# Kernel tuning notes

Hardware: AMD Instinct MI355X
Metric: run time of the kernel (lower is better)

## Reference

```python
import jax, jax.numpy as jnp
import numpy as np

BN_EPS = 1e-5
R = 8.0        # radius
L = 11         # sequence kernel size (odd), s = L//2
K = 24         # kernel_channels[-1]
N_NODES = 32768
N_EDGES = 524288
C_IN = 128     # in_channels == out_channels
C_W = 32       # width = out_channels * base_width / 64


def _bn(x, gamma, beta):
    # BatchNorm1d in training mode: biased batch statistics over node dim
    mu = jnp.mean(x, axis=0)
    var = jnp.mean(jnp.square(x - mu), axis=0)
    return (x - mu) * jax.lax.rsqrt(var + BN_EPS) * gamma + beta


def _lrelu(x, slope):
    return jnp.where(x >= 0, x, slope * x)


def setup_inputs() -> dict:
    key = jax.random.key(0)
    ks = jax.random.split(key, 10)

    def glorot(k, shape, fan_in):
        return jax.random.normal(k, shape, jnp.float32) * np.float32(1.0 / np.sqrt(fan_in))

    inp = {}
    inp["x"] = jax.random.normal(ks[0], (N_NODES, C_IN), jnp.float32)
    inp["pos"] = jax.random.normal(ks[1], (N_NODES, 3), jnp.float32) * 10.0
    inp["ori"] = jax.random.normal(ks[2], (N_NODES, 9), jnp.float32)
    inp["seq"] = jnp.arange(N_NODES, dtype=jnp.int32)
    inp["edge_index"] = jax.random.randint(ks[3], (2, N_EDGES), 0, N_NODES, jnp.int32)
    # input MLP params: BN(C_IN) -> LeakyReLU(0.1) -> Linear(C_IN->C_W, no bias) -> BN(C_W) -> LeakyReLU(0.1)
    inp["bn1_g"] = jnp.ones((C_IN,), jnp.float32)
    inp["bn1_b"] = jnp.zeros((C_IN,), jnp.float32)
    inp["lin1_w"] = glorot(ks[4], (C_IN, C_W), C_IN)
    inp["bn2_g"] = jnp.ones((C_W,), jnp.float32)
    inp["bn2_b"] = jnp.zeros((C_W,), jnp.float32)
    # CDConv WeightNet (single layer kernel_channels=[K]): per-seq-bin affine 7 -> K
    inp["wn_w"] = glorot(ks[5], (L, 7, K), 7)
    inp["wn_b"] = jnp.zeros((L, K), jnp.float32)
    # CDConv output projection: [K*C_W, C_W]
    inp["conv_w"] = glorot(ks[6], (K * C_W, C_W), K * C_W)
    # output Linear: BN(C_W) -> LeakyReLU(0.1) -> Linear(C_W->C_IN, no bias)
    inp["bn3_g"] = jnp.ones((C_W,), jnp.float32)
    inp["bn3_b"] = jnp.zeros((C_W,), jnp.float32)
    inp["lin2_w"] = glorot(ks[7], (C_W, C_IN), C_W)
    return inp


def reference(x, pos, ori, seq, edge_index,
              bn1_g, bn1_b, lin1_w, bn2_g, bn2_b,
              wn_w, wn_b, conv_w, bn3_g, bn3_b, lin2_w):
    n = x.shape[0]
    identity = x  # in_channels == out_channels -> identity branch is passthrough

    # ----- input MLP (mid_channels=None) -----
    h = _lrelu(_bn(x, bn1_g, bn1_b), 0.1)
    h = h @ lin1_w                       # [N, C_W]
    h = _lrelu(_bn(h, bn2_g, bn2_b), 0.1)

    # ----- CDConv: continuous geometric kernel over neighbor edges -----
    src, dst = edge_index[0], edge_index[1]      # message j=src -> i=dst
    d = pos[src] - pos[dst]                      # [E,3]
    dist = jnp.linalg.norm(d, axis=-1, keepdims=True)
    direction = d / (dist + 1e-9)
    Ri = ori[dst].reshape(-1, 3, 3)              # receiver local frame
    Rj = ori[src].reshape(-1, 3, 3)
    pos_local = jnp.einsum('eij,ej->ei', Ri, direction)      # direction in local frame
    ori_feat = jnp.einsum('eij,ej->ei', Ri, Rj[:, 0, :])     # neighbor axis in local frame
    delta = jnp.concatenate([pos_local, ori_feat, dist / R], axis=-1)  # [E,7]

    s = L // 2
    sidx = jnp.clip(seq[src] - seq[dst], -s, s) + s          # [E] in [0, L)

    # WeightNet: per-edge affine selected by sequence bin, LeakyReLU(0.2)
    w = _lrelu(jnp.einsum('ef,efk->ek', delta, wn_w[sidx]) + wn_b[sidx], 0.2)  # [E,K]

    # message = outer(kernel_weight, x_j), scatter-sum to receivers
    msg = (w[:, :, None] * h[src][:, None, :]).reshape(w.shape[0], K * C_W)   # [E, K*C_W]
    agg = jax.ops.segment_sum(msg, dst, num_segments=n)                        # [N, K*C_W]
    h = agg @ conv_w                                                            # [N, C_W]

    # ----- output Linear + residual -----
    h = _lrelu(_bn(h, bn3_g, bn3_b), 0.1)
    out = h @ lin2_w + identity
    return out
```

## Files before the change

kernel.cpp:

```cpp
#include <hip/hip_runtime.h>

#define N_NODES 32768
#define C_IN 128
#define C_W 32
#define KK 24
#define SS 5
#define NPB 8
#define TC 256
#define AGS (KK * C_W + 4)
#define WNS 172
#define WBS 28
#define HS 36

#define BF_LO(u) __uint_as_float((u) << 16)
#define BF_HI(u) __uint_as_float((u) & 0xFFFF0000u)

__device__ __forceinline__ unsigned int bf16pair(float lo, float hi) {
    unsigned int ulo = __float_as_uint(lo);
    unsigned int uhi = __float_as_uint(hi);
    ulo = (ulo + 0x7FFFu + ((ulo >> 16) & 1u)) >> 16;
    uhi = (uhi + 0x7FFFu + ((uhi >> 16) & 1u)) & 0xFFFF0000u;
    return uhi | ulo;
}

__global__ void __launch_bounds__(256) k_pre(
        const float* __restrict__ x, float* __restrict__ s1,
        const int* __restrict__ ei, int E, int* __restrict__ counts) {
    int t = threadIdx.x;
    int c = t % C_IN;
    int r0 = blockIdx.x * 2 + t / C_IN;
    float s = 0.f, sq = 0.f;
    for (int r = r0; r < N_NODES; r += 1024) {
        float v = x[(size_t)r * C_IN + c];
        s += v; sq += v * v;
    }
    atomicAdd(&s1[c], s);
    atomicAdd(&s1[C_IN + c], sq);
    for (int e = blockIdx.x * 256 + t; e < E; e += 512 * 256)
        atomicAdd(&counts[ei[E + e]], 1);
}

__global__ void __launch_bounds__(256) k_mlp1(
        const float* __restrict__ x, const float* __restrict__ s1,
        const float* __restrict__ g1, const float* __restrict__ b1,
        const float* __restrict__ w1, float* __restrict__ hpre,
        float* __restrict__ s2sh) {
    __shared__ float sAB[2][C_IN];
    __shared__ float sx[32][C_IN + 4];
    __shared__ float sw[C_IN][C_W];
    const int t = threadIdx.x;
    const int row0 = blockIdx.x * 32;
    if (t < C_IN) {
        float mean = s1[t] * (1.f / N_NODES);
        float var = s1[C_IN + t] * (1.f / N_NODES) - mean * mean;
        float a = g1[t] * rsqrtf(var + 1e-5f);
        sAB[0][t] = a; sAB[1][t] = b1[t] - mean * a;
    }
    for (int idx = t; idx < C_IN * C_W; idx += 256)
        sw[idx / C_W][idx % C_W] = w1[idx];
    __syncthreads();
    for (int idx = t; idx < 32 * 32; idx += 256) {
        int r = idx >> 5, cq = idx & 31;
        float4 v = *(const float4*)&x[(size_t)(row0 + r) * C_IN + cq * 4];
        float* d = &sx[r][cq * 4];
        float a0 = sAB[0][cq*4+0]*v.x + sAB[1][cq*4+0];
        float a1 = sAB[0][cq*4+1]*v.y + sAB[1][cq*4+1];
        float a2 = sAB[0][cq*4+2]*v.z + sAB[1][cq*4+2];
        float a3 = sAB[0][cq*4+3]*v.w + sAB[1][cq*4+3];
        d[0] = a0 >= 0.f ? a0 : 0.1f * a0;
        d[1] = a1 >= 0.f ? a1 : 0.1f * a1;
        d[2] = a2 >= 0.f ? a2 : 0.1f * a2;
        d[3] = a3 >= 0.f ? a3 : 0.1f * a3;
    }
    __syncthreads();
    const int r = t >> 3, c0 = (t & 7) * 4;
    float ac0 = 0.f, ac1 = 0.f, ac2 = 0.f, ac3 = 0.f;
    #pragma unroll 8
    for (int cc = 0; cc < C_IN; ++cc) {
        float xv = sx[r][cc];
        float4 wv = *(const float4*)&sw[cc][c0];
        ac0 += xv * wv.x; ac1 += xv * wv.y; ac2 += xv * wv.z; ac3 += xv * wv.w;
    }
    float4 o; o.x = ac0; o.y = ac1; o.z = ac2; o.w = ac3;
    *(float4*)&hpre[(size_t)(row0 + r) * C_W + c0] = o;
    __syncthreads();
    sx[r][c0] = ac0; sx[r][c0+1] = ac1; sx[r][c0+2] = ac2; sx[r][c0+3] = ac3;
    __syncthreads();
    if (t < C_W) {
        float s = 0.f, sq = 0.f;
        #pragma unroll
        for (int rr = 0; rr < 32; ++rr) {
            float v = sx[rr][t];
            s += v; sq += v * v;
        }
        int sh = (blockIdx.x & 7) * 64;
        atomicAdd(&s2sh[sh + t], s);
        atomicAdd(&s2sh[sh + C_W + t], sq);
    }
}

__global__ void __launch_bounds__(1024) k_scan(
        const int* __restrict__ counts, int* __restrict__ offsets,
        int* __restrict__ cursor) {
    __shared__ int sblk[1024];
    const int t = threadIdx.x;
    const int base = t * 32;
    const int4* cp = (const int4*)(counts + base);
    int loc[32];
    int s = 0;
    #pragma unroll
    for (int q = 0; q < 8; ++q) {
        int4 v = cp[q];
        loc[q*4+0] = s; s += v.x;
        loc[q*4+1] = s; s += v.y;
        loc[q*4+2] = s; s += v.z;
        loc[q*4+3] = s; s += v.w;
    }
    sblk[t] = s;
    __syncthreads();
    for (int d = 1; d < 1024; d <<= 1) {
        int u = (t >= d) ? sblk[t - d] : 0;
        __syncthreads();
        sblk[t] += u;
        __syncthreads();
    }
    const int blockbase = sblk[t] - s;
    #pragma unroll
    for (int q = 0; q < 8; ++q) {
        int4 o;
        o.x = blockbase + loc[q*4+0];
        o.y = blockbase + loc[q*4+1];
        o.z = blockbase + loc[q*4+2];
        o.w = blockbase + loc[q*4+3];
        ((int4*)(offsets + base))[q] = o;
        ((int4*)(cursor + base))[q] = o;
    }
    if (t == 1023) offsets[N_NODES] = sblk[1023];
}

__global__ void __launch_bounds__(256) k_scatter(
        const int* __restrict__ ei, int E, int* __restrict__ cursor,
        int* __restrict__ srcPerm) {
    int e = blockIdx.x * 256 + threadIdx.x;
    if (e < E) {
        int dst = ei[E + e];
        int p = atomicAdd(&cursor[dst], 1);
        srcPerm[p] = ei[e];
    }
}

__global__ void __launch_bounds__(512) k_mega(
    const int* __restrict__ offsets, const int* __restrict__ srcPerm,
    const float* __restrict__ pos, const float* __restrict__ ori,
    const int* __restrict__ seq, const float* __restrict__ hpre,
    const float* __restrict__ s2sh, const float* __restrict__ g2,
    const float* __restrict__ b2,
    const float* __restrict__ wnw, const float* __restrict__ wnb,
    const float* __restrict__ convw,
    float* __restrict__ convout, float* __restrict__ s3sh) {

    __shared__ float sWnw[11 * WNS];
    __shared__ float sWnb[11 * WBS];
    __shared__ float sA2[C_W], sB2[C_W];
    __shared__ int   sOff[NPB + 1];
    __shared__ float sNd[NPB][13];
    __shared__ union SU {
        struct { unsigned short h[TC * HS]; unsigned int w[TC * 12]; } stg;
        struct { float agg[NPB][AGS]; float red[8][NPB][C_W];
                 float rv[NPB][C_W]; float rq[NPB][C_W]; } fin;
    } U;

    const int t = threadIdx.x;
    const int i0 = blockIdx.x * NPB;
    for (int idx = t; idx < 11 * 168; idx += 512)
        sWnw[(idx / 168) * WNS + idx % 168] = wnw[idx];
    for (int idx = t; idx < 11 * 24; idx += 512)
        sWnb[(idx / 24) * WBS + idx % 24] = wnb[idx];
    if (t < C_W) {
        float s = 0.f, sq = 0.f;
        #pragma unroll
        for (int j = 0; j < 8; ++j) {
            s  += s2sh[j * 64 + t];
            sq += s2sh[j * 64 + C_W + t];
        }
        float mean = s * (1.f / N_NODES);
        float var = sq * (1.f / N_NODES) - mean * mean;
        float a = g2[t] * rsqrtf(var + 1e-5f);
        sA2[t] = a; sB2[t] = b2[t] - mean * a;
    }
    if (t <= NPB) sOff[t] = offsets[i0 + t];
    if (t < NPB * 13) {
        int n = t / 13, f = t % 13;
        float v;
        if (f < 3)       v = pos[(i0 + n) * 3 + f];
        else if (f < 12) v = ori[(i0 + n) * 9 + (f - 3)];
        else             v = __int_as_float(seq[i0 + n]);
        sNd[n][f] = v;
    }
    __syncthreads();

    const int w = t >> 6, lane = t & 63, c = lane & 31, s = lane >> 5;
    const int beg = sOff[w], end = sOff[w + 1];
    const int blkBeg = sOff[0], blkEnd = sOff[NPB];
    float a[KK];
    #pragma unroll
    for (int k = 0; k < KK; ++k) a[k] = 0.f;

    for (int base = blkBeg; base < blkEnd; base += TC) {
        const int cnt = min(TC, blkEnd - base);
        __syncthreads();
        {
            const int e    = t & 255;
            const int half = t >> 8;
            if (e < cnt) {
                const int slot = base + e;
                int g = 0;
                #pragma unroll
                for (int j = 1; j < NPB; ++j) g += (slot >= sOff[j]);
                const int src = srcPerm[slot];
                float px = pos[src*3+0], py = pos[src*3+1], pz = pos[src*3+2];
                float o0 = ori[src*9+0], o1 = ori[src*9+1], o2 = ori[src*9+2];
                int sqs = seq[src];
                float dx = px - sNd[g][0], dy = py - sNd[g][1], dz = pz - sNd[g][2];
                float dist = sqrtf(dx*dx + dy*dy + dz*dz);
                float inv = 1.f / (dist + 1e-9f);
                float ux = dx*inv, uy = dy*inv, uz = dz*inv;
                float df[7];
                #pragma unroll
                for (int r = 0; r < 3; ++r) {
                    float m0 = sNd[g][3 + r*3 + 0];
                    float m1 = sNd[g][3 + r*3 + 1];
                    float m2 = sNd[g][3 + r*3 + 2];
                    df[r]     = m0*ux + m1*uy + m2*uz;
                    df[3 + r] = m0*o0 + m1*o1 + m2*o2;
                }
                df[6] = dist * 0.125f;
                int dsq = sqs - __float_as_int(sNd[g][12]);
                dsq = dsq < -SS ? -SS : (dsq > SS ? SS : dsq);
                const int sb = dsq + SS;
                float wv[12];
                {
                    const float* wb = &sWnb[sb * WBS + half * 12];
                    #pragma unroll
                    for (int j = 0; j < 12; ++j) wv[j] = wb[j];
                }
                const float* wn = &sWnw[sb * WNS + half * 12];
                #pragma unroll
                for (int f = 0; f < 7; ++f) {
                    float d_ = df[f];
                    #pragma unroll
                    for (int j = 0; j < 12; ++j)
                        wv[j] += d_ * wn[f * 24 + j];
                }
                #pragma unroll
                for (int j = 0; j < 12; ++j) wv[j] = wv[j] >= 0.f ? wv[j] : 0.2f * wv[j];
                #pragma unroll
                for (int jj = 0; jj < 6; ++jj)
                    U.stg.w[e * 12 + half * 6 + jj] = bf16pair(wv[2*jj], wv[2*jj+1]);
                const float4* hs = (const float4*)(hpre + (size_t)src * C_W);
                uint2* hd = (uint2*)&U.stg.h[e * HS + half * 16];
                #pragma unroll
                for (int q = 0; q < 2; ++q) {
                    float4 v0 = hs[half * 4 + 2*q], v1 = hs[half * 4 + 2*q + 1];
                    float f[8] = {v0.x, v0.y, v0.z, v0.w, v1.x, v1.y, v1.z, v1.w};
                    #pragma unroll
                    for (int j = 0; j < 8; ++j) {
                        int ch = half * 16 + q * 8 + j;
                        float av = sA2[ch] * f[j] + sB2[ch];
                        f[j] = av >= 0.f ? av : 0.1f * av;
                    }
                    uint2 p0; p0.x = bf16pair(f[0], f[1]); p0.y = bf16pair(f[2], f[3]);
                    uint2 p1; p1.x = bf16pair(f[4], f[5]); p1.y = bf16pair(f[6], f[7]);
                    hd[2*q] = p0; hd[2*q+1] = p1;
                }
            }
        }
        __syncthreads();
        const int lo = max(beg, base), hi = min(end, base + cnt);
        #pragma unroll 2
        for (int p = lo + s; p < hi; p += 2) {
            const int pr = p - base;
            const float v = BF_LO((unsigned int)U.stg.h[pr * HS + c]);
            const uint4* wp = (const uint4*)&U.stg.w[pr * 12];
            const uint4 A = wp[0], B = wp[1], Cc = wp[2];
            a[0]  += BF_LO(A.x) * v;  a[1]  += BF_HI(A.x) * v;
            a[2]  += BF_LO(A.y) * v;  a[3]  += BF_HI(A.y) * v;
            a[4]  += BF_LO(A.z) * v;  a[5]  += BF_HI(A.z) * v;
            a[6]  += BF_LO(A.w) * v;  a[7]  += BF_HI(A.w) * v;
            a[8]  += BF_LO(B.x) * v;  a[9]  += BF_HI(B.x) * v;
            a[10] += BF_LO(B.y) * v;  a[11] += BF_HI(B.y) * v;
            a[12] += BF_LO(B.z) * v;  a[13] += BF_HI(B.z) * v;
            a[14] += BF_LO(B.w) * v;  a[15] += BF_HI(B.w) * v;
            a[16] += BF_LO(Cc.x) * v; a[17] += BF_HI(Cc.x) * v;
            a[18] += BF_LO(Cc.y) * v; a[19] += BF_HI(Cc.y) * v;
            a[20] += BF_LO(Cc.z) * v; a[21] += BF_HI(Cc.z) * v;
            a[22] += BF_LO(Cc.w) * v; a[23] += BF_HI(Cc.w) * v;
        }
    }
    __syncthreads();
    #pragma unroll
    for (int k = 0; k < KK; ++k) a[k] += __shfl_xor(a[k], 32, 64);
    if (s == 0) {
        #pragma unroll
        for (int k = 0; k < KK; ++k) U.fin.agg[w][k * C_W + c] = a[k];
    }
    __syncthreads();

    {
        const int coq = t & 7;
        const int gp  = (t >> 3) & 7;
        const int sl  = t >> 6;
        const int r0  = sl * 96;
        float4 acc; acc.x = acc.y = acc.z = acc.w = 0.f;
        #pragma unroll 6
        for (int rc = 0; rc < 96; rc += 4) {
            const float4 s4 = *(const float4*)&U.fin.agg[gp][r0 + rc];
            const float4 w0 = *(const float4*)&convw[(size_t)(r0+rc+0)*32 + coq*4];
            const float4 w1 = *(const float4*)&convw[(size_t)(r0+rc+1)*32 + coq*4];
            const float4 w2 = *(const float4*)&convw[(size_t)(r0+rc+2)*32 + coq*4];
            const float4 w3 = *(const float4*)&convw[(size_t)(r0+rc+3)*32 + coq*4];
            acc.x += s4.x*w0.x + s4.y*w1.x + s4.z*w2.x + s4.w*w3.x;
            acc.y += s4.x*w0.y + s4.y*w1.y + s4.z*w2.y + s4.w*w3.y;
            acc.z += s4.x*w0.z + s4.y*w1.z + s4.z*w2.z + s4.w*w3.z;
            acc.w += s4.x*w0.w + s4.y*w1.w + s4.z*w2.w + s4.w*w3.w;
        }
        *(float4*)&U.fin.red[sl][gp][coq * 4] = acc;
    }
    __syncthreads();
    if (t < 256) {
        const int gg = t >> 5, co = t & 31;
        float v = 0.f;
        #pragma unroll
        for (int sl = 0; sl < 8; ++sl) v += U.fin.red[sl][gg][co];
        convout[(size_t)(i0 + gg) * C_W + co] = v;
        U.fin.rv[gg][co] = v; U.fin.rq[gg][co] = v * v;
    }
    __syncthreads();
    if (t < 64) {
        int cc = t & 31;
        bool isq = t >= C_W;
        float s2 = 0.f;
        #pragma unroll
        for (int gg = 0; gg < NPB; ++gg)
            s2 += isq ? U.fin.rq[gg][cc] : U.fin.rv[gg][cc];
        atomicAdd(&s3sh[(blockIdx.x & 7) * 64 + t], s2);
    }
}

__global__ void __launch_bounds__(256) k_out(
        const float* __restrict__ conv, const float* __restrict__ s3sh,
        const float* __restrict__ g3, const float* __restrict__ b3,
        const float* __restrict__ w2, const float* __restrict__ x,
        float* __restrict__ out) {
    __shared__ float sAB[2][C_W];
    __shared__ float sh[8][C_W];
    __shared__ float sw2[C_W][C_IN];
    const int t = threadIdx.x;
    const int row0 = blockIdx.x * 8;
    if (t < C_W) {
        float s = 0.f, sq = 0.f;
        #pragma unroll
        for (int j = 0; j < 8; ++j) {
            s  += s3sh[j * 64 + t];
            sq += s3sh[j * 64 + C_W + t];
        }
        float mean = s * (1.f / N_NODES);
        float var = sq * (1.f / N_NODES) - mean * mean;
        float a = g3[t] * rsqrtf(var + 1e-5f);
        sAB[0][t] = a; sAB[1][t] = b3[t] - mean * a;
    }
    for (int idx = t; idx < C_W * C_IN; idx += 256)
        sw2[idx >> 7][idx & 127] = w2[idx];
    __syncthreads();
    {
        float v = conv[(size_t)row0 * C_W + t];
        int r = t >> 5, cc = t & 31;
        v = sAB[0][cc] * v + sAB[1][cc];
        sh[r][cc] = v >= 0.f ? v : 0.1f * v;
    }
    __syncthreads();
    const int r = t >> 5, c4 = (t & 31) * 4;
    float4 acc = *(const float4*)&x[(size_t)(row0 + r) * C_IN + c4];
    #pragma unroll 8
    for (int cw = 0; cw < C_W; ++cw) {
        float hv = sh[r][cw];
        float4 wv = *(const float4*)&sw2[cw][c4];
        acc.x += hv * wv.x; acc.y += hv * wv.y;
        acc.z += hv * wv.z; acc.w += hv * wv.w;
    }
    *(float4*)&out[(size_t)(row0 + r) * C_IN + c4] = acc;
}

extern "C" void kernel_launch(void* const* d_in, const int* in_sizes, int n_in,
                              void* d_out, int out_size, void* d_ws, size_t ws_size,
                              hipStream_t stream) {
    const float* x     = (const float*)d_in[0];
    const float* pos   = (const float*)d_in[1];
    const float* ori   = (const float*)d_in[2];
    const int*   seq   = (const int*)d_in[3];
    const int*   ei    = (const int*)d_in[4];
    const float* bn1g  = (const float*)d_in[5];
    const float* bn1b  = (const float*)d_in[6];
    const float* lin1w = (const float*)d_in[7];
    const float* bn2g  = (const float*)d_in[8];
    const float* bn2b  = (const float*)d_in[9];
    const float* wnw   = (const float*)d_in[10];
    const float* wnb   = (const float*)d_in[11];
    const float* convw = (const float*)d_in[12];
    const float* bn3g  = (const float*)d_in[13];
    const float* bn3b  = (const float*)d_in[14];
    const float* lin2w = (const float*)d_in[15];
    float* out = (float*)d_out;
    const int E = in_sizes[4] / 2;

    char* wsb = (char*)d_ws;
    size_t off = 0;
    auto alloc = [&](size_t bytes) {
        void* p = wsb + off;
        off = (off + bytes + 255) & ~(size_t)255;
        return p;
    };
    float* s1      = (float*)alloc(256 * 4);
    float* s2sh    = (float*)alloc(512 * 4);
    float* s3sh    = (float*)alloc(512 * 4);
    int*   counts  = (int*)alloc((size_t)N_NODES * 4);
    size_t zero_bytes = off;
    int*   offsets = (int*)alloc(((size_t)N_NODES + 1) * 4);
    int*   cursor  = (int*)alloc((size_t)N_NODES * 4);
    int*   srcPerm = (int*)alloc((size_t)E * 4);
    float* hpre    = (float*)alloc((size_t)N_NODES * C_W * 4);
    float* convo   = (float*)alloc((size_t)N_NODES * C_W * 4);

    hipMemsetAsync(wsb, 0, zero_bytes, stream);

    k_pre<<<512, 256, 0, stream>>>(x, s1, ei, E, counts);
    k_scan<<<1, 1024, 0, stream>>>(counts, offsets, cursor);
    k_scatter<<<(E + 255) / 256, 256, 0, stream>>>(ei, E, cursor, srcPerm);
    k_mlp1<<<N_NODES / 32, 256, 0, stream>>>(x, s1, bn1g, bn1b, lin1w, hpre, s2sh);
    k_mega<<<N_NODES / NPB, 512, 0, stream>>>(offsets, srcPerm, pos, ori, seq,
                                              hpre, s2sh, bn2g, bn2b, wnw, wnb,
                                              convw, convo, s3sh);
    k_out<<<N_NODES / 8, 256, 0, stream>>>(convo, s3sh, bn3g, bn3b, lin2w, x, out);
}
```

Baseline: 265.8 us.

## Split scan into multi-block passes, merge scatter with MLP1, shrink mega LDS

Replaces the single-block 1024-thread scan with a three-kernel hierarchical scan (per-block scan, block-sum scan, add offsets), so the prefix sum runs on 32 blocks instead of one. The edge scatter and the input MLP are merged into one launch, with blocks partitioned by index, so they can run at the same time. In the main kernel, the weight-net tables and node data move into the LDS union alongside the staging buffers, which cuts shared-memory use and may allow more resident blocks. Its final conv projection now reduces within each wavefront using shuffles instead of an LDS reduction plus an extra barrier. The cost is more kernel launches for the scan, plus a heterogeneous fused kernel whose two halves differ in shared memory and work.

After: 282.1 us. 1.06x slower.

```diff
diff --git a/kernel.cpp b/kernel.cpp
--- a/kernel.cpp
+++ b/kernel.cpp
@@ -40,16 +40,73 @@
         atomicAdd(&counts[ei[E + e]], 1);
 }
 
-__global__ void __launch_bounds__(256) k_mlp1(
+__global__ void __launch_bounds__(1024) k_scan1(
+        const int* __restrict__ counts, int* __restrict__ scanned,
+        int* __restrict__ blockSums) {
+    __shared__ int s[1024];
+    int t = threadIdx.x;
+    int i = blockIdx.x * 1024 + t;
+    int v = counts[i];
+    s[t] = v;
+    __syncthreads();
+    for (int d = 1; d < 1024; d <<= 1) {
+        int u = (t >= d) ? s[t - d] : 0;
+        __syncthreads();
+        s[t] += u;
+        __syncthreads();
+    }
+    scanned[i] = s[t] - v;
+    if (t == 1023) blockSums[blockIdx.x] = s[1023];
+}
+
+__global__ void k_scan2(const int* __restrict__ blockSums, int* __restrict__ blockOff,
+                        int* __restrict__ offsets) {
+    __shared__ int s[32];
+    int t = threadIdx.x;
+    int v = blockSums[t];
+    s[t] = v;
+    __syncthreads();
+    for (int d = 1; d < 32; d <<= 1) {
+        int u = (t >= d) ? s[t - d] : 0;
+        __syncthreads();
+        s[t] += u;
+        __syncthreads();
+    }
+    blockOff[t] = s[t] - v;
+    if (t == 31) offsets[N_NODES] = s[31];
+}
+
+__global__ void __launch_bounds__(1024) k_scan3(
+        const int* __restrict__ scanned, const int* __restrict__ blockOff,
+        int* __restrict__ offsets, int* __restrict__ cursor) {
+    int t = threadIdx.x;
+    int i = blockIdx.x * 1024 + t;
+    int v = scanned[i] + blockOff[blockIdx.x];
+    offsets[i] = v;
+    cursor[i] = v;
+}
+
+__global__ void __launch_bounds__(256) k_mid(
+        const int* __restrict__ ei, int E, int* __restrict__ cursor,
+        int* __restrict__ srcPerm, int SB,
         const float* __restrict__ x, const float* __restrict__ s1,
         const float* __restrict__ g1, const float* __restrict__ b1,
         const float* __restrict__ w1, float* __restrict__ hpre,
         float* __restrict__ s2sh) {
+    const int t = threadIdx.x;
+    if ((int)blockIdx.x < SB) {
+        int e = blockIdx.x * 256 + t;
+        if (e < E) {
+            int dst = ei[E + e];
+            int p = atomicAdd(&cursor[dst], 1);
+            srcPerm[p] = ei[e];
+        }
+        return;
+    }
     __shared__ float sAB[2][C_IN];
     __shared__ float sx[32][C_IN + 4];
     __shared__ float sw[C_IN][C_W];
-    const int t = threadIdx.x;
-    const int row0 = blockIdx.x * 32;
+    const int row0 = (blockIdx.x - SB) * 32;
     if (t < C_IN) {
         float mean = s1[t] * (1.f / N_NODES);
         float var = s1[C_IN + t] * (1.f / N_NODES) - mean * mean;
@@ -93,59 +150,9 @@
             float v = sx[rr][t];
             s += v; sq += v * v;
         }
-        int sh = (blockIdx.x & 7) * 64;
+        int sh = ((blockIdx.x - SB) & 7) * 64;
         atomicAdd(&s2sh[sh + t], s);
         atomicAdd(&s2sh[sh + C_W + t], sq);
-    }
-}
-
-__global__ void __launch_bounds__(1024) k_scan(
-        const int* __restrict__ counts, int* __restrict__ offsets,
-        int* __restrict__ cursor) {
-    __shared__ int sblk[1024];
-    const int t = threadIdx.x;
-    const int base = t * 32;
-    const int4* cp = (const int4*)(counts + base);
-    int loc[32];
-    int s = 0;
-    #pragma unroll
-    for (int q = 0; q < 8; ++q) {
-        int4 v = cp[q];
-        loc[q*4+0] = s; s += v.x;
-        loc[q*4+1] = s; s += v.y;
-        loc[q*4+2] = s; s += v.z;
-        loc[q*4+3] = s; s += v.w;
-    }
-    sblk[t] = s;
-    __syncthreads();
-    for (int d = 1; d < 1024; d <<= 1) {
-        int u = (t >= d) ? sblk[t - d] : 0;
-        __syncthreads();
-        sblk[t] += u;
-        __syncthreads();
-    }
-    const int blockbase = sblk[t] - s;
-    #pragma unroll
-    for (int q = 0; q < 8; ++q) {
-        int4 o;
-        o.x = blockbase + loc[q*4+0];
-        o.y = blockbase + loc[q*4+1];
-        o.z = blockbase + loc[q*4+2];
-        o.w = blockbase + loc[q*4+3];
-        ((int4*)(offsets + base))[q] = o;
-        ((int4*)(cursor + base))[q] = o;
-    }
-    if (t == 1023) offsets[N_NODES] = sblk[1023];
-}
-
-__global__ void __launch_bounds__(256) k_scatter(
-        const int* __restrict__ ei, int E, int* __restrict__ cursor,
-        int* __restrict__ srcPerm) {
-    int e = blockIdx.x * 256 + threadIdx.x;
-    if (e < E) {
-        int dst = ei[E + e];
-        int p = atomicAdd(&cursor[dst], 1);
-        srcPerm[p] = ei[e];
     }
 }
 
@@ -159,23 +166,29 @@
     const float* __restrict__ convw,
     float* __restrict__ convout, float* __restrict__ s3sh) {
 
-    __shared__ float sWnw[11 * WNS];
-    __shared__ float sWnb[11 * WBS];
-    __shared__ float sA2[C_W], sB2[C_W];
-    __shared__ int   sOff[NPB + 1];
-    __shared__ float sNd[NPB][13];
+    __shared__ int sOff[NPB + 1];
     __shared__ union SU {
-        struct { unsigned short h[TC * HS]; unsigned int w[TC * 12]; } stg;
-        struct { float agg[NPB][AGS]; float red[8][NPB][C_W];
-                 float rv[NPB][C_W]; float rq[NPB][C_W]; } fin;
+        struct {
+            float wnw[11 * WNS];
+            float wnb[11 * WBS];
+            float a2[C_W], b2[C_W];
+            float nd[NPB][13];
+            unsigned short h[TC * HS];
+            unsigned int w[TC * 12];
+        } pa;
+        struct {
+            float agg[NPB][AGS];
+            float rv[NPB][C_W];
+            float rq[NPB][C_W];
+        } fin;
     } U;
 
     const int t = threadIdx.x;
     const int i0 = blockIdx.x * NPB;
     for (int idx = t; idx < 11 * 168; idx += 512)
-        sWnw[(idx / 168) * WNS + idx % 168] = wnw[idx];
+        U.pa.wnw[(idx / 168) * WNS + idx % 168] = wnw[idx];
     for (int idx = t; idx < 11 * 24; idx += 512)
-        sWnb[(idx / 24) * WBS + idx % 24] = wnb[idx];
+        U.pa.wnb[(idx / 24) * WBS + idx % 24] = wnb[idx];
     if (t < C_W) {
         float s = 0.f, sq = 0.f;
         #pragma unroll
@@ -186,7 +199,7 @@
         float mean = s * (1.f / N_NODES);
         float var = sq * (1.f / N_NODES) - mean * mean;
         float a = g2[t] * rsqrtf(var + 1e-5f);
-        sA2[t] = a; sB2[t] = b2[t] - mean * a;
+        U.pa.a2[t] = a; U.pa.b2[t] = b2[t] - mean * a;
     }
     if (t <= NPB) sOff[t] = offsets[i0 + t];
     if (t < NPB * 13) {
@@ -195,7 +208,7 @@
         if (f < 3)       v = pos[(i0 + n) * 3 + f];
         else if (f < 12) v = ori[(i0 + n) * 9 + (f - 3)];
         else             v = __int_as_float(seq[i0 + n]);
-        sNd[n][f] = v;
+        U.pa.nd[n][f] = v;
     }
     __syncthreads();
 
@@ -221,30 +234,30 @@
                 float px = pos[src*3+0], py = pos[src*3+1], pz = pos[src*3+2];
                 float o0 = ori[src*9+0], o1 = ori[src*9+1], o2 = ori[src*9+2];
                 int sqs = seq[src];
-                float dx = px - sNd[g][0], dy = py - sNd[g][1], dz = pz - sNd[g][2];
+                float dx = px - U.pa.nd[g][0], dy = py - U.pa.nd[g][1], dz = pz - U.pa.nd[g][2];
                 float dist = sqrtf(dx*dx + dy*dy + dz*dz);
                 float inv = 1.f / (dist + 1e-9f);
                 float ux = dx*inv, uy = dy*inv, uz = dz*inv;
                 float df[7];
                 #pragma unroll
                 for (int r = 0; r < 3; ++r) {
-                    float m0 = sNd[g][3 + r*3 + 0];
-                    float m1 = sNd[g][3 + r*3 + 1];
-                    float m2 = sNd[g][3 + r*3 + 2];
+                    float m0 = U.pa.nd[g][3 + r*3 + 0];
+                    float m1 = U.pa.nd[g][3 + r*3 + 1];
+                    float m2 = U.pa.nd[g][3 + r*3 + 2];
                     df[r]     = m0*ux + m1*uy + m2*uz;
                     df[3 + r] = m0*o0 + m1*o1 + m2*o2;
                 }
                 df[6] = dist * 0.125f;
-                int dsq = sqs - __float_as_int(sNd[g][12]);
+                int dsq = sqs - __float_as_int(U.pa.nd[g][12]);
                 dsq = dsq < -SS ? -SS : (dsq > SS ? SS : dsq);
                 const int sb = dsq + SS;
                 float wv[12];
                 {
-                    const float* wb = &sWnb[sb * WBS + half * 12];
+                    const float* wb = &U.pa.wnb[sb * WBS + half * 12];
                     #pragma unroll
                     for (int j = 0; j < 12; ++j) wv[j] = wb[j];
                 }
-                const float* wn = &sWnw[sb * WNS + half * 12];
+                const float* wn = &U.pa.wnw[sb * WNS + half * 12];
                 #pragma unroll
                 for (int f = 0; f < 7; ++f) {
                     float d_ = df[f];
@@ -256,22 +269,22 @@
                 for (int j = 0; j < 12; ++j) wv[j] = wv[j] >= 0.f ? wv[j] : 0.2f * wv[j];
                 #pragma unroll
                 for (int jj = 0; jj < 6; ++jj)
-                    U.stg.w[e * 12 + half * 6 + jj] = bf16pair(wv[2*jj], wv[2*jj+1]);
+                    U.pa.w[e * 12 + half * 6 + jj] = bf16pair(wv[2*jj], wv[2*jj+1]);
                 const float4* hs = (const float4*)(hpre + (size_t)src * C_W);
-                uint2* hd = (uint2*)&U.stg.h[e * HS + half * 16];
-                #pragma unroll
-                for (int q = 0; q < 2; ++q) {
-                    float4 v0 = hs[half * 4 + 2*q], v1 = hs[half * 4 + 2*q + 1];
+                uint2* hd = (uint2*)&U.pa.h[e * HS + half * 16];
+                #pragma unroll
+                for (int g4 = 0; g4 < 2; ++g4) {
+                    float4 v0 = hs[half * 4 + 2*g4], v1 = hs[half * 4 + 2*g4 + 1];
                     float f[8] = {v0.x, v0.y, v0.z, v0.w, v1.x, v1.y, v1.z, v1.w};
                     #pragma unroll
                     for (int j = 0; j < 8; ++j) {
-                        int ch = half * 16 + q * 8 + j;
-                        float av = sA2[ch] * f[j] + sB2[ch];
+                        int ch = half * 16 + g4 * 8 + j;
+                        float av = U.pa.a2[ch] * f[j] + U.pa.b2[ch];
                         f[j] = av >= 0.f ? av : 0.1f * av;
                     }
                     uint2 p0; p0.x = bf16pair(f[0], f[1]); p0.y = bf16pair(f[2], f[3]);
                     uint2 p1; p1.x = bf16pair(f[4], f[5]); p1.y = bf16pair(f[6], f[7]);
-                    hd[2*q] = p0; hd[2*q+1] = p1;
+                    hd[2*g4] = p0; hd[2*g4+1] = p1;
                 }
             }
         }
@@ -280,8 +293,8 @@
         #pragma unroll 2
         for (int p = lo + s; p < hi; p += 2) {
             const int pr = p - base;
-            const float v = BF_LO((unsigned int)U.stg.h[pr * HS + c]);
-            const uint4* wp = (const uint4*)&U.stg.w[pr * 12];
+            const float v = BF_LO((unsigned int)U.pa.h[pr * HS + c]);
+            const uint4* wp = (const uint4*)&U.pa.w[pr * 12];
             const uint4 A = wp[0], B = wp[1], Cc = wp[2];
             a[0]  += BF_LO(A.x) * v;  a[1]  += BF_HI(A.x) * v;
             a[2]  += BF_LO(A.y) * v;  a[3]  += BF_HI(A.y) * v;
@@ -307,14 +320,14 @@
     __syncthreads();
 
     {
-        const int coq = t & 7;
-        const int gp  = (t >> 3) & 7;
-        const int sl  = t >> 6;
+        const int sl  = lane >> 3;
+        const int coq = lane & 7;
         const int r0  = sl * 96;
         float4 acc; acc.x = acc.y = acc.z = acc.w = 0.f;
-        #pragma unroll 6
-        for (int rc = 0; rc < 96; rc += 4) {
-            const float4 s4 = *(const float4*)&U.fin.agg[gp][r0 + rc];
+        #pragma unroll 4
+        for (int j = 0; j < 24; ++j) {
+            const int rc = ((j + sl * 3) % 24) * 4;
+            const float4 s4 = *(const float4*)&U.fin.agg[w][r0 + rc];
             const float4 w0 = *(const float4*)&convw[(size_t)(r0+rc+0)*32 + coq*4];
             const float4 w1 = *(const float4*)&convw[(size_t)(r0+rc+1)*32 + coq*4];
             const float4 w2 = *(const float4*)&convw[(size_t)(r0+rc+2)*32 + coq*4];
@@ -324,16 +337,20 @@
             acc.z += s4.x*w0.z + s4.y*w1.z + s4.z*w2.z + s4.w*w3.z;
             acc.w += s4.x*w0.w + s4.y*w1.w + s4.z*w2.w + s4.w*w3.w;
         }
-        *(float4*)&U.fin.red[sl][gp][coq * 4] = acc;
-    }
-    __syncthreads();
-    if (t < 256) {
-        const int gg = t >> 5, co = t & 31;
-        float v = 0.f;
-        #pragma unroll
-        for (int sl = 0; sl < 8; ++sl) v += U.fin.red[sl][gg][co];
-        convout[(size_t)(i0 + gg) * C_W + co] = v;
-        U.fin.rv[gg][co] = v; U.fin.rq[gg][co] = v * v;
+        #pragma unroll
+        for (int d = 8; d <= 32; d <<= 1) {
+            acc.x += __shfl_xor(acc.x, d, 64);
+            acc.y += __shfl_xor(acc.y, d, 64);
+            acc.z += __shfl_xor(acc.z, d, 64);
+            acc.w += __shfl_xor(acc.w, d, 64);
+        }
+        if (lane < 8) {
+            *(float4*)&convout[(size_t)(i0 + w) * C_W + coq * 4] = acc;
+            float4 sq; sq.x = acc.x*acc.x; sq.y = acc.y*acc.y;
+            sq.z = acc.z*acc.z; sq.w = acc.w*acc.w;
+            *(float4*)&U.fin.rv[w][coq * 4] = acc;
+            *(float4*)&U.fin.rq[w][coq * 4] = sq;
+        }
     }
     __syncthreads();
     if (t < 64) {
@@ -425,6 +442,9 @@
     float* s3sh    = (float*)alloc(512 * 4);
     int*   counts  = (int*)alloc((size_t)N_NODES * 4);
     size_t zero_bytes = off;
+    int*   scanned = (int*)alloc((size_t)N_NODES * 4);
+    int*   bsums   = (int*)alloc(64 * 4);
+    int*   boff    = (int*)alloc(64 * 4);
     int*   offsets = (int*)alloc(((size_t)N_NODES + 1) * 4);
     int*   cursor  = (int*)alloc((size_t)N_NODES * 4);
     int*   srcPerm = (int*)alloc((size_t)E * 4);
@@ -433,10 +453,14 @@
 
     hipMemsetAsync(wsb, 0, zero_bytes, stream);
 
+    const int SB = (E + 255) / 256;
     k_pre<<<512, 256, 0, stream>>>(x, s1, ei, E, counts);
-    k_scan<<<1, 1024, 0, stream>>>(counts, offsets, cursor);
-    k_scatter<<<(E + 255) / 256, 256, 0, stream>>>(ei, E, cursor, srcPerm);
-    k_mlp1<<<N_NODES / 32, 256, 0, stream>>>(x, s1, bn1g, bn1b, lin1w, hpre, s2sh);
+    k_scan1<<<32, 1024, 0, stream>>>(counts, scanned, bsums);
+    k_scan2<<<1, 32, 0, stream>>>(bsums, boff, offsets);
+    k_scan3<<<32, 1024, 0, stream>>>(scanned, boff, offsets, cursor);
+    k_mid<<<SB + N_NODES / 32, 256, 0, stream>>>(ei, E, cursor, srcPerm, SB,
+                                                 x, s1, bn1g, bn1b, lin1w,
+                                                 hpre, s2sh);
     k_mega<<<N_NODES / NPB, 512, 0, stream>>>(offsets, srcPerm, pos, ori, seq,
                                               hpre, s2sh, bn2g, bn2b, wnw, wnb,
                                               convw, convo, s3sh);
```
